# Kernel optimization log

Measured on AMD Instinct MI355X. Metric: run time of the kernel, lower is better.

The kernel has to match this reference:

```python
import jax, jax.numpy as jnp
import numpy as np

NEG_SLOPE = 0.2  # PyG GATConv default negative_slope
EPS = 1e-16      # PyG softmax denominator epsilon


def gat_conv(x, W, att_src, att_dst, bias, src, dst, num_nodes, concat):
    H, C = att_src.shape
    h = (x @ W).reshape(-1, H, C)                    # [N,H,C]
    a_src = jnp.einsum('nhc,hc->nh', h, att_src)      # [N,H]
    a_dst = jnp.einsum('nhc,hc->nh', h, att_dst)      # [N,H]
    e = a_src[src] + a_dst[dst]                       # [E,H]
    e = jax.nn.leaky_relu(e, NEG_SLOPE)
    # segment softmax over incoming edges of each destination node
    e_max = jax.ops.segment_max(e, dst, num_segments=num_nodes)   # [N,H]
    e_max = jnp.where(jnp.isfinite(e_max), e_max, 0.0)
    p = jnp.exp(e - e_max[dst])                        # [E,H]
    denom = jax.ops.segment_sum(p, dst, num_segments=num_nodes)   # [N,H]
    alpha = p / (denom[dst] + EPS)                     # [E,H]
    msg = h[src] * alpha[:, :, None]                   # [E,H,C]
    out = jax.ops.segment_sum(msg, dst, num_segments=num_nodes)   # [N,H,C]
    if concat:
        out = out.reshape(num_nodes, H * C)
    else:
        out = out.mean(axis=1)
    return out + bias


def setup_inputs() -> dict:
    key = jax.random.key(0)
    ks = jax.random.split(key, 10)
    N, E, Fin, H, C, OUT = 50000, 400000, 128, 8, 32, 32
    s = 0.05
    return {
        'x': jax.random.normal(ks[0], (N, Fin), jnp.float32),
        'edge_index': jax.random.randint(ks[1], (2, E), 0, N, jnp.int64),
        'W1': jax.random.normal(ks[2], (Fin, H * C), jnp.float32) * s,
        'att_src1': jax.random.normal(ks[3], (H, C), jnp.float32) * s,
        'att_dst1': jax.random.normal(ks[4], (H, C), jnp.float32) * s,
        'b1': jax.random.normal(ks[5], (H * C,), jnp.float32) * s,
        'W2': jax.random.normal(ks[6], (H * C, H * OUT), jnp.float32) * s,
        'att_src2': jax.random.normal(ks[7], (H, OUT), jnp.float32) * s,
        'att_dst2': jax.random.normal(ks[8], (H, OUT), jnp.float32) * s,
        'b2': jax.random.normal(ks[9], (OUT,), jnp.float32) * s,
    }


def reference(x, edge_index, W1, att_src1, att_dst1, b1, W2, att_src2, att_dst2, b2):
    N = x.shape[0]
    src, dst = edge_index[0], edge_index[1]
    h = gat_conv(x, W1, att_src1, att_dst1, b1, src, dst, N, concat=True)
    h = jax.nn.elu(h)  # dropout p=0 / eval: identity
    out = gat_conv(h, W2, att_src2, att_dst2, b2, src, dst, N, concat=False)
    return out
```

## Files before the change

### kernel.cpp

```cpp
#include <hip/hip_runtime.h>
#include <math.h>

#define NEG_SLOPE 0.2f

typedef float f32x4 __attribute__((ext_vector_type(4)));
typedef short bf16x8 __attribute__((ext_vector_type(8)));
typedef unsigned short ushortv8 __attribute__((ext_vector_type(8)));

__device__ __forceinline__ unsigned short f2bf(float f) {
    union { float f; unsigned u; } uu; uu.f = f;
    unsigned r = uu.u + 0x7FFF + ((uu.u >> 16) & 1);
    return (unsigned short)(r >> 16);
}
__device__ __forceinline__ float bf2f(unsigned short u) {
    union { unsigned u; float f; } x; x.u = ((unsigned)u) << 16; return x.f;
}

__global__ void prep_kernel(const float* __restrict__ W1, unsigned short* __restrict__ Wt1,
                            const float* __restrict__ W2, unsigned short* __restrict__ Wt2,
                            int* __restrict__ counts, int* __restrict__ cursor, int N)
{
    int u = blockIdx.x * 256 + threadIdx.x;
    if (u < 32768) {
        int nn = u >> 7, k = u & 127;
        Wt1[u] = f2bf(W1[(size_t)k * 256 + nn]);
        return;
    }
    u -= 32768;
    if (u < 65536) {
        int nn = u >> 8, k = u & 255;
        Wt2[u] = f2bf(W2[(size_t)k * 256 + nn]);
        return;
    }
    u -= 65536;
    if (u < N) { counts[u] = 0; cursor[u] = 0; }
}

__global__ void hist_kernel(const int* __restrict__ dst, int* __restrict__ counts, int E)
{
    int e = blockIdx.x * 256 + threadIdx.x;
    if (e < E) atomicAdd(&counts[dst[e]], 1);
}

template<int CVT>
__global__ __launch_bounds__(512) void gemm_mfma(
    const void* __restrict__ Av,
    const unsigned short* __restrict__ Bt,
    unsigned short* __restrict__ C,
    const float* __restrict__ att_s,
    const float* __restrict__ att_d,
    float* __restrict__ a_s,
    float* __restrict__ a_d,
    int M, int K, int gemmBlocks,
    const int* __restrict__ srcp, const int* __restrict__ dstp,
    const int* __restrict__ incl, const int* __restrict__ bsum,
    int* __restrict__ rowptr, int* __restrict__ cursor,
    int* __restrict__ esrc, int E)
{
    __shared__ unsigned short As[128 * 64];
    __shared__ unsigned short Bs[256 * 64];

    if ((int)blockIdx.x >= gemmBlocks) {
        int t = ((int)blockIdx.x - gemmBlocks) * 512 + threadIdx.x;
        int Nn = M;
        if (t < Nn) {
            rowptr[t + 1] = incl[t] + bsum[t >> 8];
            if (t == 0) rowptr[0] = 0;
        }
        if (t < E) {
            int d = dstp[t];
            int rp = bsum[d >> 8] + ((d & 255) ? incl[d - 1] : 0);
            int pos = rp + atomicAdd(&cursor[d], 1);
            esrc[pos] = srcp[t];
        }
        return;
    }

    const int tid  = threadIdx.x;
    const int lane = tid & 63;
    const int wave = tid >> 6;
    const int wr = wave >> 2, wc = wave & 3;
    const int row0 = blockIdx.x * 128;

    f32x4 acc[4][4] = {};
    ushortv8 va[2], vb[4];

    auto load_tile = [&](int k0) {
        #pragma unroll
        for (int i = 0; i < 2; ++i) {
            int c  = i * 512 + tid;
            int r  = c >> 3, cc = c & 7;
            int ga = row0 + r; if (ga >= M) ga = M - 1;
            if constexpr (CVT) {
                const float* ap = (const float*)Av + (size_t)ga * K + k0 + cc * 8;
                float4 lo = *(const float4*)ap;
                float4 hi = *(const float4*)(ap + 4);
                ushortv8 o;
                o[0]=f2bf(lo.x); o[1]=f2bf(lo.y); o[2]=f2bf(lo.z); o[3]=f2bf(lo.w);
                o[4]=f2bf(hi.x); o[5]=f2bf(hi.y); o[6]=f2bf(hi.z); o[7]=f2bf(hi.w);
                va[i] = o;
            } else {
                va[i] = *(const ushortv8*)((const unsigned short*)Av +
                                           (size_t)ga * K + k0 + cc * 8);
            }
        }
        #pragma unroll
        for (int i = 0; i < 4; ++i) {
            int c  = i * 512 + tid;
            int r  = c >> 3, cc = c & 7;
            vb[i] = *(const ushortv8*)(Bt + (size_t)r * K + k0 + cc * 8);
        }
    };

    load_tile(0);

    for (int k0 = 0; k0 < K; k0 += 64) {
        __syncthreads();
        #pragma unroll
        for (int i = 0; i < 2; ++i) {
            int c  = i * 512 + tid;
            int r  = c >> 3, cc = c & 7;
            *(ushortv8*)(As + r * 64 + (cc ^ (r & 7)) * 8) = va[i];
        }
        #pragma unroll
        for (int i = 0; i < 4; ++i) {
            int c  = i * 512 + tid;
            int r  = c >> 3, cc = c & 7;
            *(ushortv8*)(Bs + r * 64 + (cc ^ (r & 7)) * 8) = vb[i];
        }
        __syncthreads();

        if (k0 + 64 < K) load_tile(k0 + 64);
        #pragma unroll
        for (int kk = 0; kk < 2; ++kk) {
            const int kbyte = kk * 64 + ((lane >> 4) << 4);
            bf16x8 af[4], bfr[4];
            #pragma unroll
            for (int m = 0; m < 4; ++m) {
                int r = wr * 64 + m * 16 + (lane & 15);
                af[m] = *(const bf16x8*)((const char*)As + r * 128 + (kbyte ^ ((r & 7) << 4)));
            }
            #pragma unroll
            for (int n = 0; n < 4; ++n) {
                int r = wc * 64 + n * 16 + (lane & 15);
                bfr[n] = *(const bf16x8*)((const char*)Bs + r * 128 + (kbyte ^ ((r & 7) << 4)));
            }
            #pragma unroll
            for (int m = 0; m < 4; ++m)
                #pragma unroll
                for (int n = 0; n < 4; ++n)
                    acc[m][n] = __builtin_amdgcn_mfma_f32_16x16x32_bf16(
                        af[m], bfr[n], acc[m][n], 0, 0, 0);
        }
    }

    #pragma unroll
    for (int m = 0; m < 4; ++m) {
        int rbase = row0 + wr * 64 + m * 16 + ((lane >> 4) << 2);
        #pragma unroll
        for (int j = 0; j < 4; ++j) {
            int grow = rbase + j;
            if (grow < M) {
                #pragma unroll
                for (int n = 0; n < 4; ++n)
                    C[(size_t)grow * 256 + wc * 64 + n * 16 + (lane & 15)] =
                        f2bf(acc[m][n][j]);
            }
        }
    }

    float asv[4], adv[4];
    #pragma unroll
    for (int n = 0; n < 4; ++n) {
        int colg = wc * 64 + n * 16 + (lane & 15);
        asv[n] = att_s[colg];
        adv[n] = att_d[colg];
    }
    const int hbase = wc * 2;
    #pragma unroll
    for (int m = 0; m < 4; ++m) {
        int rbase = row0 + wr * 64 + m * 16 + ((lane >> 4) << 2);
        #pragma unroll
        for (int j = 0; j < 4; ++j) {
            int grow = rbase + j;
            #pragma unroll
            for (int t = 0; t < 2; ++t) {
                float vs = acc[m][2*t][j] * asv[2*t] + acc[m][2*t+1][j] * asv[2*t+1];
                float vd = acc[m][2*t][j] * adv[2*t] + acc[m][2*t+1][j] * adv[2*t+1];
                #pragma unroll
                for (int off = 1; off < 16; off <<= 1) {
                    vs += __shfl_xor(vs, off);
                    vd += __shfl_xor(vd, off);
                }
                if ((lane & 15) == 0 && grow < M) {
                    a_s[(size_t)grow * 8 + hbase + t] = vs;
                    a_d[(size_t)grow * 8 + hbase + t] = vd;
                }
            }
        }
    }
}

__global__ __launch_bounds__(256) void scan_blk(
    const int* __restrict__ counts, int* __restrict__ incl, int* __restrict__ bsum, int N)
{
    __shared__ int wtot[4], wexc[4];
    int t = blockIdx.x * 256 + threadIdx.x;
    int lane = threadIdx.x & 63, wid = threadIdx.x >> 6;
    int v = (t < N) ? counts[t] : 0;
    int s = v;
    #pragma unroll
    for (int off = 1; off < 64; off <<= 1) {
        int u = __shfl_up(s, off);
        if (lane >= off) s += u;
    }
    if (lane == 63) wtot[wid] = s;
    __syncthreads();
    if (threadIdx.x == 0) {
        int r = 0;
        #pragma unroll
        for (int w = 0; w < 4; ++w) { wexc[w] = r; r += wtot[w]; }
    }
    __syncthreads();
    int out = s + wexc[wid];
    if (t < N) incl[t] = out;
    if (threadIdx.x == 255) bsum[blockIdx.x] = out;
}

__global__ __launch_bounds__(256) void scan_top(int* __restrict__ bsum, int nb)
{
    __shared__ int wtot[4], wexc[4];
    int tid = threadIdx.x;
    int lane = tid & 63, wid = tid >> 6;
    int v = (tid < nb) ? bsum[tid] : 0;
    int s = v;
    #pragma unroll
    for (int off = 1; off < 64; off <<= 1) {
        int u = __shfl_up(s, off);
        if (lane >= off) s += u;
    }
    if (lane == 63) wtot[wid] = s;
    __syncthreads();
    if (tid == 0) {
        int r = 0;
        #pragma unroll
        for (int w = 0; w < 4; ++w) { wexc[w] = r; r += wtot[w]; }
    }
    __syncthreads();
    if (tid < nb) bsum[tid] = s + wexc[wid] - v;
}

template<int LAYER>
__global__ __launch_bounds__(128) void gat_agg(
    const unsigned short* __restrict__ h, const float* __restrict__ a_s,
    const float* __restrict__ a_d, const int* __restrict__ rowptr,
    const int* __restrict__ esrc, const float* __restrict__ bias,
    float* __restrict__ out, unsigned short* __restrict__ out_b, int N)
{
    const int n  = blockIdx.x * 4 + (threadIdx.x >> 5);
    if (n >= N) return;
    const int sl   = threadIdx.x & 31;
    const int head = sl >> 2;
    const int beg = rowptr[n];
    const int deg = rowptr[n + 1] - beg;

    const float adn = a_d[(size_t)n*8 + head];
    float dsum = 0.f;
    float2 acc2[4] = {{0.f,0.f},{0.f,0.f},{0.f,0.f},{0.f,0.f}};

    int j0 = 0;
    for (; j0 + 4 <= deg; j0 += 4) {
        int s0 = esrc[beg + j0 + 0];
        int s1 = esrc[beg + j0 + 1];
        int s2 = esrc[beg + j0 + 2];
        int s3 = esrc[beg + j0 + 3];
        int sv[4] = {s0, s1, s2, s3};
        #pragma unroll
        for (int k = 0; k < 4; ++k) {
            int s = sv[k];
            float e = a_s[(size_t)s*8 + head] + adn;
            e = fmaxf(e, NEG_SLOPE * e);
            float p = __expf(e);
            dsum += p;
            uint4 hv = *(const uint4*)(h + (size_t)s*256 + sl*8);
            const unsigned* hw = (const unsigned*)&hv;
            #pragma unroll
            for (int i = 0; i < 4; ++i) {
                acc2[i].x += p * __uint_as_float(hw[i] << 16);
                acc2[i].y += p * __uint_as_float(hw[i] & 0xffff0000u);
            }
        }
    }
    for (; j0 < deg; ++j0) {
        int s = esrc[beg + j0];
        float e = a_s[(size_t)s*8 + head] + adn;
        e = fmaxf(e, NEG_SLOPE * e);
        float p = __expf(e);
        dsum += p;
        uint4 hv = *(const uint4*)(h + (size_t)s*256 + sl*8);
        const unsigned* hw = (const unsigned*)&hv;
        #pragma unroll
        for (int i = 0; i < 4; ++i) {
            acc2[i].x += p * __uint_as_float(hw[i] << 16);
            acc2[i].y += p * __uint_as_float(hw[i] & 0xffff0000u);
        }
    }

    float invd = 1.f / (dsum + 1e-16f);

    if (LAYER == 1) {
        ushortv8 o;
        #pragma unroll
        for (int i = 0; i < 4; ++i) {
            float v0 = acc2[i].x * invd + bias[sl*8 + 2*i];
            float v1 = acc2[i].y * invd + bias[sl*8 + 2*i + 1];
            o[2*i]   = f2bf(v0 > 0.f ? v0 : expf(v0) - 1.f);
            o[2*i+1] = f2bf(v1 > 0.f ? v1 : expf(v1) - 1.f);
        }
        *(ushortv8*)(out_b + (size_t)n*256 + sl*8) = o;
    } else {
        #pragma unroll
        for (int i = 0; i < 4; ++i) { acc2[i].x *= invd; acc2[i].y *= invd; }
        #pragma unroll
        for (int m = 4; m <= 16; m <<= 1)
            #pragma unroll
            for (int i = 0; i < 4; ++i) {
                acc2[i].x += __shfl_xor(acc2[i].x, m);
                acc2[i].y += __shfl_xor(acc2[i].y, m);
            }
        if (sl < 4) {
            float4 lo = make_float4(acc2[0].x*0.125f + bias[sl*8+0],
                                    acc2[0].y*0.125f + bias[sl*8+1],
                                    acc2[1].x*0.125f + bias[sl*8+2],
                                    acc2[1].y*0.125f + bias[sl*8+3]);
            float4 hi = make_float4(acc2[2].x*0.125f + bias[sl*8+4],
                                    acc2[2].y*0.125f + bias[sl*8+5],
                                    acc2[3].x*0.125f + bias[sl*8+6],
                                    acc2[3].y*0.125f + bias[sl*8+7]);
            *(float4*)(out + (size_t)n*32 + sl*8)     = lo;
            *(float4*)(out + (size_t)n*32 + sl*8 + 4) = hi;
        }
    }
}

extern "C" void kernel_launch(void* const* d_in, const int* in_sizes, int n_in,
                              void* d_out, int out_size, void* d_ws, size_t ws_size,
                              hipStream_t stream)
{
    const float* x   = (const float*)d_in[0];
    const int*   ei  = (const int*)  d_in[1];
    const float* W1  = (const float*)d_in[2];
    const float* as1 = (const float*)d_in[3];
    const float* ad1 = (const float*)d_in[4];
    const float* b1  = (const float*)d_in[5];
    const float* W2  = (const float*)d_in[6];
    const float* as2 = (const float*)d_in[7];
    const float* ad2 = (const float*)d_in[8];
    const float* b2  = (const float*)d_in[9];

    const int N = in_sizes[0] / 128;
    const int E = in_sizes[1] / 2;
    const int* srcp = ei;
    const int* dstp = ei + E;

    char* ws = (char*)d_ws;
    unsigned short* hb    = (unsigned short*)ws;  ws += (size_t)N * 256 * 2;
    unsigned short* out1b = (unsigned short*)ws;  ws += (size_t)N * 256 * 2;
    unsigned short* Wt1   = (unsigned short*)ws;  ws += 256 * 128 * 2;
    unsigned short* Wt2   = (unsigned short*)ws;  ws += 256 * 256 * 2;
    float*          a_s   = (float*)ws;           ws += (size_t)N * 8 * 4;
    float*          a_d   = (float*)ws;           ws += (size_t)N * 8 * 4;
    int*            counts= (int*)ws;             ws += (size_t)N * 4;
    int*            cursor= (int*)ws;             ws += (size_t)N * 4;
    int*            incl  = (int*)ws;             ws += (size_t)N * 4;
    int*            bsum  = (int*)ws;             ws += 256 * 4;
    int*            rowptr= (int*)ws;             ws += (size_t)(N + 1) * 4;
    int*            esrc  = (int*)ws;

    const int nb = (N + 255) / 256;

    {
        int tot = 32768 + 65536 + N;
        prep_kernel<<<(tot + 255) / 256, 256, 0, stream>>>(
            W1, Wt1, W2, Wt2, counts, cursor, N);
    }
    hist_kernel<<<(E + 255) / 256, 256, 0, stream>>>(dstp, counts, E);
    scan_blk<<<nb, 256, 0, stream>>>(counts, incl, bsum, N);
    scan_top<<<1, 256, 0, stream>>>(bsum, nb);

    const int gridM = (N + 127) / 128;
    const int fillB = (E + 511) / 512;

    gemm_mfma<1><<<gridM + fillB, 512, 0, stream>>>(
        x, Wt1, hb, as1, ad1, a_s, a_d, N, 128, gridM,
        srcp, dstp, incl, bsum, rowptr, cursor, esrc, E);
    gat_agg<1><<<(N + 3) / 4, 128, 0, stream>>>(hb, a_s, a_d, rowptr, esrc, b1,
                                                nullptr, out1b, N);

    gemm_mfma<0><<<gridM, 512, 0, stream>>>(
        out1b, Wt2, hb, as2, ad2, a_s, a_d, N, 256, gridM,
        srcp, dstp, incl, bsum, rowptr, cursor, esrc, E);
    gat_agg<2><<<(N + 3) / 4, 128, 0, stream>>>(hb, a_s, a_d, rowptr, esrc, b2,
                                                (float*)d_out, nullptr, N);
}
```

Measured before the change: 170.3 us.

## Drop LDS staging in MFMA GEMM, load fragments directly from global memory

The GEMM no longer stages tiles through shared memory with barriers. Each wave now loads its MFMA A and B fragments straight from global memory, with K fixed as a template parameter so the K loop fully unrolls. The block shrinks to 64 rows by 256 columns with 256 threads. This removes the LDS writes, reads and syncthreads, at the cost of redundant global and L2 reads because the four waves each reload the same A rows and B is reread by every block. The fused CSR-fill tail blocks are resized to match.

```diff
diff --git a/kernel.cpp b/kernel.cpp
--- a/kernel.cpp
+++ b/kernel.cpp
@@ -42,8 +42,8 @@
     if (e < E) atomicAdd(&counts[dst[e]], 1);
 }
 
-template<int CVT>
-__global__ __launch_bounds__(512) void gemm_mfma(
+template<int CVT, int KC>
+__global__ __launch_bounds__(256) void gemm_mfma(
     const void* __restrict__ Av,
     const unsigned short* __restrict__ Bt,
     unsigned short* __restrict__ C,
@@ -51,19 +51,15 @@
     const float* __restrict__ att_d,
     float* __restrict__ a_s,
     float* __restrict__ a_d,
-    int M, int K, int gemmBlocks,
+    int M, int gemmBlocks,
     const int* __restrict__ srcp, const int* __restrict__ dstp,
     const int* __restrict__ incl, const int* __restrict__ bsum,
     int* __restrict__ rowptr, int* __restrict__ cursor,
     int* __restrict__ esrc, int E)
 {
-    __shared__ unsigned short As[128 * 64];
-    __shared__ unsigned short Bs[256 * 64];
-
     if ((int)blockIdx.x >= gemmBlocks) {
-        int t = ((int)blockIdx.x - gemmBlocks) * 512 + threadIdx.x;
-        int Nn = M;
-        if (t < Nn) {
+        int t = ((int)blockIdx.x - gemmBlocks) * 256 + threadIdx.x;
+        if (t < M) {
             rowptr[t + 1] = incl[t] + bsum[t >> 8];
             if (t == 0) rowptr[0] = 0;
         }
@@ -78,92 +74,63 @@
 
     const int tid  = threadIdx.x;
     const int lane = tid & 63;
-    const int wave = tid >> 6;
-    const int wr = wave >> 2, wc = wave & 3;
-    const int row0 = blockIdx.x * 128;
+    const int wc   = tid >> 6;
+    const int row0 = blockIdx.x * 64;
+    const int l15  = lane & 15;
+    const int kg   = (lane >> 4) * 8;
+
+    int rowm[4];
+    #pragma unroll
+    for (int m = 0; m < 4; ++m) {
+        int r = row0 + m * 16 + l15;
+        rowm[m] = (r < M) ? r : (M - 1);
+    }
+    int coln[4];
+    #pragma unroll
+    for (int n = 0; n < 4; ++n) coln[n] = wc * 64 + n * 16 + l15;
 
     f32x4 acc[4][4] = {};
-    ushortv8 va[2], vb[4];
-
-    auto load_tile = [&](int k0) {
-        #pragma unroll
-        for (int i = 0; i < 2; ++i) {
-            int c  = i * 512 + tid;
-            int r  = c >> 3, cc = c & 7;
-            int ga = row0 + r; if (ga >= M) ga = M - 1;
+
+    #pragma unroll
+    for (int ks = 0; ks < KC / 32; ++ks) {
+        const int k = ks * 32 + kg;
+        bf16x8 af[4], bfr[4];
+        #pragma unroll
+        for (int m = 0; m < 4; ++m) {
             if constexpr (CVT) {
-                const float* ap = (const float*)Av + (size_t)ga * K + k0 + cc * 8;
+                const float* ap = (const float*)Av + (size_t)rowm[m] * KC + k;
                 float4 lo = *(const float4*)ap;
                 float4 hi = *(const float4*)(ap + 4);
                 ushortv8 o;
                 o[0]=f2bf(lo.x); o[1]=f2bf(lo.y); o[2]=f2bf(lo.z); o[3]=f2bf(lo.w);
                 o[4]=f2bf(hi.x); o[5]=f2bf(hi.y); o[6]=f2bf(hi.z); o[7]=f2bf(hi.w);
-                va[i] = o;
+                af[m] = (bf16x8)o;
             } else {
-                va[i] = *(const ushortv8*)((const unsigned short*)Av +
-                                           (size_t)ga * K + k0 + cc * 8);
-            }
-        }
-        #pragma unroll
-        for (int i = 0; i < 4; ++i) {
-            int c  = i * 512 + tid;
-            int r  = c >> 3, cc = c & 7;
-            vb[i] = *(const ushortv8*)(Bt + (size_t)r * K + k0 + cc * 8);
-        }
-    };
-
-    load_tile(0);
-
-    for (int k0 = 0; k0 < K; k0 += 64) {
-        __syncthreads();
-        #pragma unroll
-        for (int i = 0; i < 2; ++i) {
-            int c  = i * 512 + tid;
-            int r  = c >> 3, cc = c & 7;
-            *(ushortv8*)(As + r * 64 + (cc ^ (r & 7)) * 8) = va[i];
-        }
-        #pragma unroll
-        for (int i = 0; i < 4; ++i) {
-            int c  = i * 512 + tid;
-            int r  = c >> 3, cc = c & 7;
-            *(ushortv8*)(Bs + r * 64 + (cc ^ (r & 7)) * 8) = vb[i];
-        }
-        __syncthreads();
-
-        if (k0 + 64 < K) load_tile(k0 + 64);
-        #pragma unroll
-        for (int kk = 0; kk < 2; ++kk) {
-            const int kbyte = kk * 64 + ((lane >> 4) << 4);
-            bf16x8 af[4], bfr[4];
+                af[m] = *(const bf16x8*)((const unsigned short*)Av +
+                                         (size_t)rowm[m] * KC + k);
+            }
+        }
+        #pragma unroll
+        for (int n = 0; n < 4; ++n)
+            bfr[n] = *(const bf16x8*)(Bt + (size_t)coln[n] * KC + k);
+        #pragma unroll
+        for (int m = 0; m < 4; ++m)
             #pragma unroll
-            for (int m = 0; m < 4; ++m) {
-                int r = wr * 64 + m * 16 + (lane & 15);
-                af[m] = *(const bf16x8*)((const char*)As + r * 128 + (kbyte ^ ((r & 7) << 4)));
-            }
-            #pragma unroll
-            for (int n = 0; n < 4; ++n) {
-                int r = wc * 64 + n * 16 + (lane & 15);
-                bfr[n] = *(const bf16x8*)((const char*)Bs + r * 128 + (kbyte ^ ((r & 7) << 4)));
-            }
-            #pragma unroll
-            for (int m = 0; m < 4; ++m)
-                #pragma unroll
-                for (int n = 0; n < 4; ++n)
-                    acc[m][n] = __builtin_amdgcn_mfma_f32_16x16x32_bf16(
-                        af[m], bfr[n], acc[m][n], 0, 0, 0);
-        }
+            for (int n = 0; n < 4; ++n)
+                acc[m][n] = __builtin_amdgcn_mfma_f32_16x16x32_bf16(
+                    af[m], bfr[n], acc[m][n], 0, 0, 0);
     }
 
     #pragma unroll
     for (int m = 0; m < 4; ++m) {
-        int rbase = row0 + wr * 64 + m * 16 + ((lane >> 4) << 2);
+        int rbase = row0 + m * 16 + ((lane >> 4) << 2);
         #pragma unroll
         for (int j = 0; j < 4; ++j) {
             int grow = rbase + j;
             if (grow < M) {
                 #pragma unroll
                 for (int n = 0; n < 4; ++n)
-                    C[(size_t)grow * 256 + wc * 64 + n * 16 + (lane & 15)] =
+                    C[(size_t)grow * 256 + wc * 64 + n * 16 + l15] =
                         f2bf(acc[m][n][j]);
             }
         }
@@ -172,14 +139,14 @@
     float asv[4], adv[4];
     #pragma unroll
     for (int n = 0; n < 4; ++n) {
-        int colg = wc * 64 + n * 16 + (lane & 15);
+        int colg = wc * 64 + n * 16 + l15;
         asv[n] = att_s[colg];
         adv[n] = att_d[colg];
     }
     const int hbase = wc * 2;
     #pragma unroll
     for (int m = 0; m < 4; ++m) {
-        int rbase = row0 + wr * 64 + m * 16 + ((lane >> 4) << 2);
+        int rbase = row0 + m * 16 + ((lane >> 4) << 2);
         #pragma unroll
         for (int j = 0; j < 4; ++j) {
             int grow = rbase + j;
@@ -192,7 +159,7 @@
                     vs += __shfl_xor(vs, off);
                     vd += __shfl_xor(vd, off);
                 }
-                if ((lane & 15) == 0 && grow < M) {
+                if (l15 == 0 && grow < M) {
                     a_s[(size_t)grow * 8 + hbase + t] = vs;
                     a_d[(size_t)grow * 8 + hbase + t] = vd;
                 }
@@ -388,17 +355,17 @@
     scan_blk<<<nb, 256, 0, stream>>>(counts, incl, bsum, N);
     scan_top<<<1, 256, 0, stream>>>(bsum, nb);
 
-    const int gridM = (N + 127) / 128;
-    const int fillB = (E + 511) / 512;
-
-    gemm_mfma<1><<<gridM + fillB, 512, 0, stream>>>(
-        x, Wt1, hb, as1, ad1, a_s, a_d, N, 128, gridM,
+    const int gridM = (N + 63) / 64;
+    const int fillB = (E + 255) / 256;
+
+    gemm_mfma<1, 128><<<gridM + fillB, 256, 0, stream>>>(
+        x, Wt1, hb, as1, ad1, a_s, a_d, N, gridM,
         srcp, dstp, incl, bsum, rowptr, cursor, esrc, E);
     gat_agg<1><<<(N + 3) / 4, 128, 0, stream>>>(hb, a_s, a_d, rowptr, esrc, b1,
                                                 nullptr, out1b, N);
 
-    gemm_mfma<0><<<gridM, 512, 0, stream>>>(
-        out1b, Wt2, hb, as2, ad2, a_s, a_d, N, 256, gridM,
+    gemm_mfma<0, 256><<<gridM, 256, 0, stream>>>(
+        out1b, Wt2, hb, as2, ad2, a_s, a_d, N, gridM,
         srcp, dstp, incl, bsum, rowptr, cursor, esrc, E);
     gat_agg<2><<<(N + 3) / 4, 128, 0, stream>>>(hb, a_s, a_d, rowptr, esrc, b2,
                                                 (float*)d_out, nullptr, N);
```

Measured after the change: 199.0 us. 1.17x slower.
